# Performance work log

Hardware: AMD Instinct MI355X
Metric: run time of the kernel (lower is better)

Reference implementation:

```python
import jax, jax.numpy as jnp
import numpy as np

LAYERS = 2
HEADS = 4
TYPE_IDX = 1  # type='logic' -> 1
HIDDEN = 256
HEAD_DIM = HIDDEN // HEADS
EPS = 1e-6


def setup_inputs() -> dict:
    key = jax.random.key(0)
    ks = jax.random.split(key, 12)
    B, S, H = 4, 2048, HIDDEN
    inputs = jax.random.normal(ks[0], (B, S, H), jnp.float32)
    graphs = jax.random.uniform(ks[1], (B, 2, S, S), jnp.float32)
    biases_batch = jax.random.normal(ks[2], (B, 2, S, S), jnp.float32)
    s_h = 1.0 / np.sqrt(H).astype(np.float32)
    s_d = 1.0 / np.sqrt(HEAD_DIM).astype(np.float32)
    gc_w = jax.random.normal(ks[3], (LAYERS, H, H), jnp.float32) * s_h
    gc_b = jnp.zeros((LAYERS, H), jnp.float32)
    attn_w = jax.random.normal(ks[4], (LAYERS, HEAD_DIM, H), jnp.float32) * s_h  # conv1 (1x1) weight
    attn_a = jax.random.normal(ks[5], (LAYERS, HEAD_DIM), jnp.float32) * s_d     # conv2_1 (1x1) weight
    ln_a = jnp.ones((H,), jnp.float32)
    ln_b = jnp.zeros((H,), jnp.float32)
    w1 = jax.random.normal(ks[6], (H, H), jnp.float32) * s_h
    w1b = jnp.zeros((H,), jnp.float32)
    w2 = jax.random.normal(ks[7], (H, H), jnp.float32) * s_h
    w2b = jnp.zeros((H,), jnp.float32)
    return dict(inputs=inputs, graphs=graphs, biases_batch=biases_batch,
                gc_w=gc_w, gc_b=gc_b, attn_w=attn_w, attn_a=attn_a,
                ln_a=ln_a, ln_b=ln_b, w1=w1, w1b=w1b, w2=w2, w2b=w2b)


def reference(inputs, graphs, biases_batch, gc_w, gc_b, attn_w, attn_a, ln_a, ln_b, w1, w1b, w2, w2b):
    adj = graphs[:, TYPE_IDX]          # [b,s,s]
    bias = biases_batch[:, TYPE_IDX]   # [b,s,s]
    x0 = inputs
    x = inputs
    for i in range(LAYERS):
        # GraphConvolution: adj @ (x @ W) + b
        mf = jnp.einsum('bij,bjh->bih', adj, x @ gc_w[i]) + gc_b[i]
        # Node_Attn_head (NOTE: original uses conv2_1 for BOTH f_1 and f_2)
        seq_fts = jnp.einsum('bsh,dh->bsd', mf, attn_w[i])      # [b,s,d]
        f = seq_fts @ attn_a[i]                                  # [b,s]
        logits = jax.nn.leaky_relu(f[:, :, None] + f[:, None, :])  # f_2^T + f_1 -> [b,s,s]
        coefs = jax.nn.softmax(logits + bias, axis=1)            # Softmax(dim=1)
        ret = jax.nn.leaky_relu(jnp.einsum('bij,bjd->bid', coefs, seq_fts))  # [b,s,d]
        # shared attention head across all HEADS -> identical outputs, concatenated
        x = jnp.tile(ret, (1, 1, HEADS)) + x
    # LayerNorm (torch.std is unbiased -> ddof=1), residual to original inputs
    mean = x.mean(-1, keepdims=True)
    std = jnp.std(x, axis=-1, keepdims=True, ddof=1)
    g = ln_a * (x - mean) / (std + EPS) + ln_b + x0
    # PositionwiseFeedForward (dropout inactive in eval)
    ff = jax.nn.relu(g @ w1.T + w1b) @ w2.T + w2b
    return ff + g
```

## Files before the change

kernel.cpp:

```cpp
#include <hip/hip_runtime.h>
#include <math.h>

#define BB 4
#define SS 2048
#define HH 256
#define DD 64
#define NLAYERS 2
#define NPART 128

#define XSC  (1.f/64.f)
#define XSCI 64.f
#define FSC  (1.f/256.f)
#define WSC  256.f

typedef _Float16 f16;
typedef f16 half8 __attribute__((ext_vector_type(8)));
typedef f16 half4 __attribute__((ext_vector_type(4)));
typedef float f32x4 __attribute__((ext_vector_type(4)));
#define MFMA16(a, b, c) __builtin_amdgcn_mfma_f32_16x16x32_f16(a, b, c, 0, 0, 0)

__device__ __forceinline__ float lrelu(float v) { return v > 0.f ? v : 0.01f * v; }
__device__ __forceinline__ int enc(float f) { int i = __float_as_int(f); return i >= 0 ? i : (i ^ 0x7fffffff); }
__device__ __forceinline__ float dec(int k) { int i = k >= 0 ? k : (k ^ 0x7fffffff); return __int_as_float(i); }
__device__ __forceinline__ void split8(const float* v, half8& h, half8& l) {
    #pragma unroll
    for (int e = 0; e < 8; ++e) {
        f16 hh = (f16)v[e]; h[e] = hh; l[e] = (f16)((v[e] - (float)hh) * 2048.f);
    }
}

__global__ __launch_bounds__(256) void split_scale(
    const float* __restrict__ src, f16* __restrict__ dh, f16* __restrict__ dl, float scale)
{
    long i = ((long)blockIdx.x * 256 + threadIdx.x) * 8;
    float4 a = *(const float4*)&src[i];
    float4 b = *(const float4*)&src[i + 4];
    float v[8] = {a.x * scale, a.y * scale, a.z * scale, a.w * scale,
                  b.x * scale, b.y * scale, b.z * scale, b.w * scale};
    half8 h, l; split8(v, h, l);
    *(half8*)&dh[i] = h; *(half8*)&dl[i] = l;
}

__global__ __launch_bounds__(256) void prep_wy(
    const float* __restrict__ gc_w, const float* __restrict__ gc_b,
    const float* __restrict__ attn_w,
    f16* __restrict__ WysH, f16* __restrict__ WysL, float* __restrict__ by,
    const float* __restrict__ w1, const float* __restrict__ w2,
    f16* __restrict__ w1h, f16* __restrict__ w1l,
    f16* __restrict__ w2h, f16* __restrict__ w2l, int* __restrict__ FMXi)
{
    int L = blockIdx.x >> 6, d = blockIdx.x & 63;
    int h = threadIdx.x;
    const float* gw = gc_w + (long)L * HH * HH;
    const float* aw = attn_w + (long)L * DD * HH + (long)d * HH;
    float acc = 0.f;
    for (int hp = 0; hp < HH; ++hp) acc += gw[(long)h * HH + hp] * aw[hp];
    f16 hh = (f16)acc;
    WysH[((long)L * DD + d) * HH + h] = hh;
    WysL[((long)L * DD + d) * HH + h] = (f16)((acc - (float)hh) * 2048.f);
    if (h == 0) {
        float ba = 0.f;
        const float* gb = gc_b + (long)L * HH;
        for (int hp = 0; hp < HH; ++hp) ba += gb[hp] * aw[hp];
        by[L * DD + d] = ba;
    }
    int gt = blockIdx.x * 256 + h;
    #pragma unroll
    for (int p = 0; p < 4; ++p) {
        int e = gt * 4 + p;
        if (e < 65536) {
            float v = w1[e]; f16 x = (f16)v;
            w1h[e] = x; w1l[e] = (f16)((v - (float)x) * 2048.f);
        } else {
            int e2 = e - 65536;
            float v = w2[e2]; f16 x = (f16)v;
            w2h[e2] = x; w2l[e2] = (f16)((v - (float)x) * 2048.f);
        }
    }
    if (blockIdx.x == 0 && h < 2 * BB) FMXi[h] = enc(-1e30f);
}

__global__ __launch_bounds__(256) void y_mfma(
    const f16* __restrict__ xh, const f16* __restrict__ xl,
    const f16* __restrict__ WyhL, const f16* __restrict__ WylL,
    f16* __restrict__ yTh, f16* __restrict__ yTl)
{
    const int tid = threadIdx.x;
    const int w = tid >> 6, l = tid & 63;
    const int gw = blockIdx.x * 4 + w;
    const int b = gw >> 7, st = gw & 127;
    const int s0 = st * 16;
    const int lr = l & 15, kg = (l >> 4) * 8;
    const f16* Aph = xh + ((long)b * SS + s0 + lr) * HH;
    const f16* Apl = xl + ((long)b * SS + s0 + lr) * HH;
    f32x4 acch[4] = {}, accm[4] = {};
    #pragma unroll
    for (int k0 = 0; k0 < HH; k0 += 32) {
        half8 ah = *(const half8*)(Aph + k0 + kg);
        half8 al = *(const half8*)(Apl + k0 + kg);
        #pragma unroll
        for (int dt = 0; dt < 4; ++dt) {
            long boff = (long)(dt * 16 + lr) * HH + k0 + kg;
            half8 bh = *(const half8*)(WyhL + boff);
            half8 bl = *(const half8*)(WylL + boff);
            acch[dt] = MFMA16(ah, bh, acch[dt]);
            accm[dt] = MFMA16(ah, bl, accm[dt]);
            accm[dt] = MFMA16(al, bh, accm[dt]);
        }
    }
    const int rg0 = (l >> 4) * 4;
    #pragma unroll
    for (int dt = 0; dt < 4; ++dt) {
        int d = dt * 16 + lr;
        half4 h4, l4;
        #pragma unroll
        for (int rr = 0; rr < 4; ++rr) {
            float v = acch[dt][rr] + accm[dt][rr] * (1.f / 2048.f);
            f16 hh = (f16)v; h4[rr] = hh; l4[rr] = (f16)((v - (float)hh) * 2048.f);
        }
        long ob = ((long)b * DD + d) * SS + s0 + rg0;
        *(half4*)(yTh + ob) = h4;
        *(half4*)(yTl + ob) = l4;
    }
}

__global__ __launch_bounds__(512, 4) void ftp_fused(
    const float* __restrict__ adjB,
    const f16* __restrict__ yTh, const f16* __restrict__ yTl,
    const float* __restrict__ byL, const float* __restrict__ aaL,
    float* __restrict__ F, f16* __restrict__ fTh, f16* __restrict__ fTl,
    int* __restrict__ fmxSlot)
{
    __shared__ float Ls[8][16][68];
    __shared__ float fmaxS[16];
    const int b = blockIdx.y;
    const int i0 = blockIdx.x * 16;
    const int tid = threadIdx.x;
    const int w = tid >> 6, l = tid & 63, lr = l & 15, kg = (l >> 4) * 8;
    const float* Arow = adjB + (long)b * 2 * SS * SS + (long)(i0 + lr) * SS;
    const f16* Bh = yTh + ((long)b * DD + lr) * SS;
    const f16* Bl = yTl + ((long)b * DD + lr) * SS;

    f32x4 acch[4] = {}, accm[4] = {};
    #pragma unroll
    for (int ks = 0; ks < 256; ks += 32) {
        int k = w * 256 + ks + kg;
        float4 a0 = *(const float4*)(Arow + k);
        float4 a1 = *(const float4*)(Arow + k + 4);
        float av[8] = {a0.x, a0.y, a0.z, a0.w, a1.x, a1.y, a1.z, a1.w};
        half8 ah, al; split8(av, ah, al);
        #pragma unroll
        for (int dt = 0; dt < 4; ++dt) {
            long off = (long)dt * 16 * SS + k;
            half8 bh = *(const half8*)(Bh + off);
            half8 bl = *(const half8*)(Bl + off);
            acch[dt] = MFMA16(ah, bh, acch[dt]);
            accm[dt] = MFMA16(ah, bl, accm[dt]);
            accm[dt] = MFMA16(al, bh, accm[dt]);
        }
    }
    const int rg0 = (l >> 4) * 4;
    #pragma unroll
    for (int dt = 0; dt < 4; ++dt)
        #pragma unroll
        for (int rr = 0; rr < 4; ++rr)
            Ls[w][rg0 + rr][dt * 16 + lr] = acch[dt][rr] + accm[dt][rr] * (1.f / 2048.f);
    __syncthreads();

    {
        int r = tid >> 5, q = tid & 31, c0 = q * 2;
        float s0 = 0.f, s1 = 0.f;
        #pragma unroll
        for (int ww = 0; ww < 8; ++ww) { s0 += Ls[ww][r][c0]; s1 += Ls[ww][r][c0 + 1]; }
        s0 = s0 * XSCI + byL[c0];
        s1 = s1 * XSCI + byL[c0 + 1];
        Ls[0][r][c0] = s0; Ls[0][r][c0 + 1] = s1;
        float dot = s0 * aaL[c0] + s1 * aaL[c0 + 1];
        dot += __shfl_xor(dot, 1, 64);
        dot += __shfl_xor(dot, 2, 64);
        dot += __shfl_xor(dot, 4, 64);
        dot += __shfl_xor(dot, 8, 64);
        dot += __shfl_xor(dot, 16, 64);
        if (q == 0) { F[b * SS + i0 + r] = dot; fmaxS[r] = dot; }
    }
    __syncthreads();
    if (tid == 0) {
        float m = -1e30f;
        #pragma unroll
        for (int r = 0; r < 16; ++r) m = fmaxf(m, fmaxS[r]);
        atomicMax(fmxSlot + b, enc(m));
    }
    if (tid < 256) {
        int d = tid >> 2, sq = (tid & 3) * 4;
        half4 h4, l4;
        #pragma unroll
        for (int e = 0; e < 4; ++e) {
            float v = Ls[0][sq + e][d] * FSC;
            f16 hh = (f16)v; h4[e] = hh; l4[e] = (f16)((v - (float)hh) * 2048.f);
        }
        long ob = ((long)b * DD + d) * SS + i0 + sq;
        *(half4*)(fTh + ob) = h4;
        *(half4*)(fTl + ob) = l4;
    }
}

__global__ __launch_bounds__(512) void col_stats_part(
    const float* __restrict__ biasb, const float* __restrict__ f,
    const int* __restrict__ fmxSlot,
    float* __restrict__ partS, float* __restrict__ Mv)
{
    __shared__ float fs[32];
    const int b = blockIdx.z;
    const int chunk = blockIdx.y;
    const int half = threadIdx.x >> 8;
    const int t = threadIdx.x & 255;
    const int j0 = blockIdx.x * 1024 + t * 4;
    const float* bb = biasb + (long)b * 2 * SS * SS;
    const int ibase = chunk * 32 + half * 16;

    if (threadIdx.x < 32) fs[threadIdx.x] = f[b * SS + chunk * 32 + threadIdx.x];

    float fj[4], M[4], s[4] = {0.f, 0.f, 0.f, 0.f};
    const float fmx = dec(fmxSlot[b]);
    #pragma unroll
    for (int q = 0; q < 4; ++q) {
        fj[q] = f[b * SS + j0 + q];
        M[q] = lrelu(fmx + fj[q]) + 8.f;
    }
    __syncthreads();

    #pragma unroll
    for (int ii = 0; ii < 16; ii += 2) {
        float fi0 = fs[half * 16 + ii], fi1 = fs[half * 16 + ii + 1];
        float4 b0 = *(const float4*)&bb[(long)(ibase + ii) * SS + j0];
        float4 b1 = *(const float4*)&bb[(long)(ibase + ii + 1) * SS + j0];
        s[0] += __expf(lrelu(fi0 + fj[0]) + b0.x - M[0]);
        s[1] += __expf(lrelu(fi0 + fj[1]) + b0.y - M[1]);
        s[2] += __expf(lrelu(fi0 + fj[2]) + b0.z - M[2]);
        s[3] += __expf(lrelu(fi0 + fj[3]) + b0.w - M[3]);
        s[0] += __expf(lrelu(fi1 + fj[0]) + b1.x - M[0]);
        s[1] += __expf(lrelu(fi1 + fj[1]) + b1.y - M[1]);
        s[2] += __expf(lrelu(fi1 + fj[2]) + b1.z - M[2]);
        s[3] += __expf(lrelu(fi1 + fj[3]) + b1.w - M[3]);
    }
    const int c = chunk * 2 + half;
    #pragma unroll
    for (int q = 0; q < 4; ++q)
        partS[((long)c * BB + b) * SS + j0 + q] = s[q];
    if (chunk == 0 && half == 0) {
        #pragma unroll
        for (int q = 0; q < 4; ++q) Mv[b * SS + j0 + q] = M[q];
    }
}

__global__ __launch_bounds__(256) void col_stats_merge(
    const float* __restrict__ partS, float* __restrict__ Sinv)
{
    __shared__ float red[4][64];
    const int b = blockIdx.y;
    const int jl = threadIdx.x & 63;
    const int p = threadIdx.x >> 6;
    const int j = blockIdx.x * 64 + jl;
    float s = 0.f;
    #pragma unroll
    for (int k = 0; k < 32; ++k)
        s += partS[((long)(p * 32 + k) * BB + b) * SS + j];
    red[p][jl] = s;
    __syncthreads();
    if (p == 0) {
        float tot = ((red[0][jl] + red[1][jl]) + (red[2][jl] + red[3][jl]));
        Sinv[b * SS + j] = 1.f / tot;
    }
}

__global__ __launch_bounds__(512, 4) void pvp_fused(
    const float* __restrict__ biasb, const float* __restrict__ f,
    const float* __restrict__ Mv, const float* __restrict__ Sinv,
    const f16* __restrict__ fTh, const f16* __restrict__ fTl,
    const float* __restrict__ xin, float* __restrict__ X,
    f16* __restrict__ xh, f16* __restrict__ xl, int writeSplit)
{
    __shared__ float Ls[8][16][68];
    const int b = blockIdx.y;
    const int i0 = blockIdx.x * 16;
    const int tid = threadIdx.x;
    const int w = tid >> 6, l = tid & 63, lr = l & 15, kg = (l >> 4) * 8;
    const int irow = i0 + lr;
    const float fi = f[b * SS + irow];
    const float* brow = biasb + (long)b * 2 * SS * SS + (long)irow * SS;
    const float* fb = f + b * SS;
    const float* mb = Mv + b * SS;
    const float* sb = Sinv + b * SS;
    const f16* Bh = fTh + ((long)b * DD + lr) * SS;
    const f16* Bl = fTl + ((long)b * DD + lr) * SS;

    f32x4 acch[4] = {}, accm[4] = {};
    #pragma unroll
    for (int jc = 0; jc < 256; jc += 32) {
        const int jb = w * 256 + jc + kg;
        float4 bs0 = *(const float4*)(brow + jb);
        float4 bs1 = *(const float4*)(brow + jb + 4);
        float4 fj0 = *(const float4*)(fb + jb);
        float4 fj1 = *(const float4*)(fb + jb + 4);
        float4 mj0 = *(const float4*)(mb + jb);
        float4 mj1 = *(const float4*)(mb + jb + 4);
        float4 sj0 = *(const float4*)(sb + jb);
        float4 sj1 = *(const float4*)(sb + jb + 4);
        float wv[8];
        wv[0] = __expf(lrelu(fi + fj0.x) + bs0.x - mj0.x) * sj0.x * WSC;
        wv[1] = __expf(lrelu(fi + fj0.y) + bs0.y - mj0.y) * sj0.y * WSC;
        wv[2] = __expf(lrelu(fi + fj0.z) + bs0.z - mj0.z) * sj0.z * WSC;
        wv[3] = __expf(lrelu(fi + fj0.w) + bs0.w - mj0.w) * sj0.w * WSC;
        wv[4] = __expf(lrelu(fi + fj1.x) + bs1.x - mj1.x) * sj1.x * WSC;
        wv[5] = __expf(lrelu(fi + fj1.y) + bs1.y - mj1.y) * sj1.y * WSC;
        wv[6] = __expf(lrelu(fi + fj1.z) + bs1.z - mj1.z) * sj1.z * WSC;
        wv[7] = __expf(lrelu(fi + fj1.w) + bs1.w - mj1.w) * sj1.w * WSC;
        half8 ah, al; split8(wv, ah, al);
        #pragma unroll
        for (int dt = 0; dt < 4; ++dt) {
            long off = (long)dt * 16 * SS + jb;
            half8 bh = *(const half8*)(Bh + off);
            half8 bl = *(const half8*)(Bl + off);
            acch[dt] = MFMA16(ah, bh, acch[dt]);
            accm[dt] = MFMA16(ah, bl, accm[dt]);
            accm[dt] = MFMA16(al, bh, accm[dt]);
        }
    }
    const int rg0 = (l >> 4) * 4;
    #pragma unroll
    for (int dt = 0; dt < 4; ++dt)
        #pragma unroll
        for (int rr = 0; rr < 4; ++rr)
            Ls[w][rg0 + rr][dt * 16 + lr] = acch[dt][rr] + accm[dt][rr] * (1.f / 2048.f);
    __syncthreads();

    {
        int r = tid >> 5, q = tid & 31, dq = q * 2;
        float v0 = 0.f, v1 = 0.f;
        #pragma unroll
        for (int ww = 0; ww < 8; ++ww) { v0 += Ls[ww][r][dq]; v1 += Ls[ww][r][dq + 1]; }
        v0 = lrelu(v0); v1 = lrelu(v1);
        long rowoff = ((long)b * SS + i0 + r) * HH;
        #pragma unroll
        for (int rep = 0; rep < 4; ++rep) {
            long off = rowoff + rep * DD + dq;
            float o0 = v0 + xin[off];
            float o1 = v1 + xin[off + 1];
            X[off] = o0; X[off + 1] = o1;
            if (writeSplit) {
                float s0 = o0 * XSC, s1 = o1 * XSC;
                f16 h0 = (f16)s0, h1 = (f16)s1;
                xh[off] = h0; xl[off] = (f16)((s0 - (float)h0) * 2048.f);
                xh[off + 1] = h1; xl[off + 1] = (f16)((s1 - (float)h1) * 2048.f);
            }
        }
    }
}

__global__ __launch_bounds__(256) void layernorm_g(
    const float* __restrict__ x, const float* __restrict__ x0,
    const float* __restrict__ lna, const float* __restrict__ lnb,
    float* __restrict__ g, f16* __restrict__ gh, f16* __restrict__ gl)
{
    __shared__ float red[8];
    long row = blockIdx.x;
    int t = threadIdx.x;
    int wave = t >> 6, lane = t & 63;
    float v = x[row * HH + t];

    float sum = v;
    #pragma unroll
    for (int off = 32; off; off >>= 1) sum += __shfl_down(sum, off, 64);
    if (lane == 0) red[wave] = sum;
    __syncthreads();
    if (t < 64) {
        float s = (lane < 4) ? red[lane] : 0.f;
        s += __shfl_down(s, 2, 64);
        s += __shfl_down(s, 1, 64);
        if (lane == 0) red[4] = s / HH;
    }
    __syncthreads();
    float mean = red[4];
    float d = v - mean;
    float sq = d * d;
    #pragma unroll
    for (int off = 32; off; off >>= 1) sq += __shfl_down(sq, off, 64);
    __syncthreads();
    if (lane == 0) red[wave] = sq;
    __syncthreads();
    if (t < 64) {
        float s = (lane < 4) ? red[lane] : 0.f;
        s += __shfl_down(s, 2, 64);
        s += __shfl_down(s, 1, 64);
        if (lane == 0) red[5] = sqrtf(s / (HH - 1));
    }
    __syncthreads();
    float stdv = red[5];
    float gv = lna[t] * d / (stdv + 1e-6f) + lnb[t] + x0[row * HH + t];
    g[row * HH + t] = gv;
    f16 hh = (f16)gv;
    gh[row * HH + t] = hh;
    gl[row * HH + t] = (f16)((gv - (float)hh) * 2048.f);
}

__global__ __launch_bounds__(256) void ffn_mfma(
    const f16* __restrict__ Ah, const f16* __restrict__ Al,
    const f16* __restrict__ Bh, const f16* __restrict__ Bl,
    const float* __restrict__ bias, const float* __restrict__ res,
    float* __restrict__ outF, f16* __restrict__ outH, f16* __restrict__ outL,
    int doRelu)
{
    __shared__ float Ls[64][68];
    const int i0 = blockIdx.x * 64, j0 = blockIdx.y * 64;
    const int tid = threadIdx.x;
    const int w = tid >> 6, l = tid & 63, lr = l & 15, kg = (l >> 4) * 8;
    const f16* Aph = Ah + ((long)i0 + w * 16 + lr) * HH;
    const f16* Apl = Al + ((long)i0 + w * 16 + lr) * HH;
    f32x4 acch[4] = {}, accm[4] = {};
    #pragma unroll
    for (int k0 = 0; k0 < HH; k0 += 32) {
        half8 ah = *(const half8*)(Aph + k0 + kg);
        half8 al = *(const half8*)(Apl + k0 + kg);
        #pragma unroll
        for (int dt = 0; dt < 4; ++dt) {
            long boff = ((long)(j0 + dt * 16 + lr)) * HH + k0 + kg;
            half8 bh = *(const half8*)(Bh + boff);
            half8 bl = *(const half8*)(Bl + boff);
            acch[dt] = MFMA16(ah, bh, acch[dt]);
            accm[dt] = MFMA16(ah, bl, accm[dt]);
            accm[dt] = MFMA16(al, bh, accm[dt]);
        }
    }
    const int rg0 = (l >> 4) * 4;
    #pragma unroll
    for (int dt = 0; dt < 4; ++dt) {
        float bj = bias[j0 + dt * 16 + lr];
        #pragma unroll
        for (int rr = 0; rr < 4; ++rr) {
            float v = acch[dt][rr] + accm[dt][rr] * (1.f / 2048.f) + bj;
            if (doRelu) v = fmaxf(v, 0.f);
            Ls[w * 16 + rg0 + rr][dt * 16 + lr] = v;
        }
    }
    __syncthreads();
    int s = tid >> 2, nq = (tid & 3) * 16;
    long go = ((long)i0 + s) * HH + j0 + nq;
    if (outF) {
        #pragma unroll
        for (int q = 0; q < 4; ++q) {
            float4 v = *(float4*)&Ls[s][nq + q * 4];
            if (res) {
                float4 r = *(const float4*)&res[go + q * 4];
                v.x += r.x; v.y += r.y; v.z += r.z; v.w += r.w;
            }
            *(float4*)&outF[go + q * 4] = v;
        }
    } else {
        float v0[8], v1[8];
        #pragma unroll
        for (int e = 0; e < 8; ++e) { v0[e] = Ls[s][nq + e]; v1[e] = Ls[s][nq + 8 + e]; }
        half8 h0, l0, h1, l1; split8(v0, h0, l0); split8(v1, h1, l1);
        *(half8*)&outH[go] = h0; *(half8*)&outH[go + 8] = h1;
        *(half8*)&outL[go] = l0; *(half8*)&outL[go + 8] = l1;
    }
}

extern "C" void kernel_launch(void* const* d_in, const int* in_sizes, int n_in,
                              void* d_out, int out_size, void* d_ws, size_t ws_size,
                              hipStream_t stream)
{
    const float* inputs = (const float*)d_in[0];
    const float* graphs = (const float*)d_in[1];
    const float* biases = (const float*)d_in[2];
    const float* gc_w   = (const float*)d_in[3];
    const float* gc_b   = (const float*)d_in[4];
    const float* attn_w = (const float*)d_in[5];
    const float* attn_a = (const float*)d_in[6];
    const float* ln_a   = (const float*)d_in[7];
    const float* ln_b   = (const float*)d_in[8];
    const float* w1     = (const float*)d_in[9];
    const float* w1b    = (const float*)d_in[10];
    const float* w2     = (const float*)d_in[11];
    const float* w2b    = (const float*)d_in[12];
    float* out = (float*)d_out;

    float* ws   = (float*)d_ws;
    float* X    = ws;
    float* G    = ws + 2097152;
    float* PTS  = ws + 4194304;
    float* F    = ws + 5242880;
    float* Mv   = ws + 5251072;
    float* Sv   = ws + 5259264;
    float* by   = ws + 5267456;
    int*   FMXi = (int*)(ws + 5267584);
    f16* WysH   = (f16*)(ws + 5267712);
    f16* WysL   = (f16*)(ws + 5284096);
    f16* yTh    = (f16*)(ws + 5300480);
    f16* yTl    = (f16*)(ws + 5562624);
    f16* fTh    = (f16*)(ws + 5824768);
    f16* fTl    = (f16*)(ws + 6086912);
    f16* xh     = (f16*)(ws + 6349056);
    f16* xl     = (f16*)(ws + 7397632);
    f16* gh     = (f16*)(ws + 8446208);
    f16* gl     = (f16*)(ws + 9494784);
    f16* h1h    = (f16*)(ws + 10543360);
    f16* h1l    = (f16*)(ws + 11591936);
    f16* w1h    = (f16*)(ws + 12640512);
    f16* w1l    = (f16*)(ws + 12673280);
    f16* w2h    = (f16*)(ws + 12706048);
    f16* w2l    = (f16*)(ws + 12738816);

    const float* adjBase  = graphs + (long)SS * SS;
    const float* biasBase = biases + (long)SS * SS;

    prep_wy<<<128, 256, 0, stream>>>(gc_w, gc_b, attn_w, WysH, WysL, by,
                                     w1, w2, w1h, w1l, w2h, w2l, FMXi);
    split_scale<<<1024, 256, 0, stream>>>(inputs, xh, xl, XSC);

    for (int L = 0; L < NLAYERS; ++L) {
        y_mfma<<<128, 256, 0, stream>>>(xh, xl,
            WysH + (long)L * DD * HH, WysL + (long)L * DD * HH, yTh, yTl);
        ftp_fused<<<dim3(128, BB), 512, 0, stream>>>(
            adjBase, yTh, yTl, by + L * DD, attn_a + (long)L * DD,
            F, fTh, fTl, FMXi + L * BB);
        col_stats_part<<<dim3(2, 64, BB), 512, 0, stream>>>(
            biasBase, F, FMXi + L * BB, PTS, Mv);
        col_stats_merge<<<dim3(32, BB), 256, 0, stream>>>(PTS, Sv);
        pvp_fused<<<dim3(128, BB), 512, 0, stream>>>(
            biasBase, F, Mv, Sv, fTh, fTl,
            (L == 0) ? inputs : X, X, xh, xl, (L == 0) ? 1 : 0);
    }

    layernorm_g<<<BB * SS, 256, 0, stream>>>(X, inputs, ln_a, ln_b, G, gh, gl);
    ffn_mfma<<<dim3(128, 4), 256, 0, stream>>>(gh, gl, w1h, w1l, w1b,
                                               nullptr, nullptr, h1h, h1l, 1);
    ffn_mfma<<<dim3(128, 4), 256, 0, stream>>>(h1h, h1l, w2h, w2l, w2b,
                                               G, out, nullptr, nullptr, 0);
}
```

Before: 311.2 us.

## Fold softmax normalizer into log-space offset, wave-per-row layernorm, vectorize prep

The column max, the 1/sum and the fp16 scale are folded into a single per-column log-space offset (log 256 - log sum - max), so pvp_fused streams one vector instead of two and drops two multiplies per element. LayerNorm now handles one row per wavefront with float4 loads and xor shuffles, removing shared-memory reductions and barriers. prep_wy's dot product is vectorized with float4. The launch bounds of ftp_fused and pvp_fused drop from 4 to 2 blocks per CU, which gives the compiler more registers at the cost of occupancy.

Result: faster. 303.8 us (-2.4%).

```diff
diff --git a/kernel.cpp b/kernel.cpp
--- a/kernel.cpp
+++ b/kernel.cpp
@@ -12,6 +12,7 @@
 #define XSCI 64.f
 #define FSC  (1.f/256.f)
 #define WSC  256.f
+#define LNWSC 5.5451774444795624f
 
 typedef _Float16 f16;
 typedef f16 half8 __attribute__((ext_vector_type(8)));
@@ -51,10 +52,15 @@
 {
     int L = blockIdx.x >> 6, d = blockIdx.x & 63;
     int h = threadIdx.x;
-    const float* gw = gc_w + (long)L * HH * HH;
+    const float* gwr = gc_w + (long)L * HH * HH + (long)h * HH;
     const float* aw = attn_w + (long)L * DD * HH + (long)d * HH;
     float acc = 0.f;
-    for (int hp = 0; hp < HH; ++hp) acc += gw[(long)h * HH + hp] * aw[hp];
+    #pragma unroll 4
+    for (int hp = 0; hp < HH; hp += 4) {
+        float4 g4 = *(const float4*)&gwr[hp];
+        float4 a4 = *(const float4*)&aw[hp];
+        acc += g4.x * a4.x + g4.y * a4.y + g4.z * a4.z + g4.w * a4.w;
+    }
     f16 hh = (f16)acc;
     WysH[((long)L * DD + d) * HH + h] = hh;
     WysL[((long)L * DD + d) * HH + h] = (f16)((acc - (float)hh) * 2048.f);
@@ -124,7 +130,7 @@
     }
 }
 
-__global__ __launch_bounds__(512, 4) void ftp_fused(
+__global__ __launch_bounds__(512, 2) void ftp_fused(
     const float* __restrict__ adjB,
     const f16* __restrict__ yTh, const f16* __restrict__ yTl,
     const float* __restrict__ byL, const float* __restrict__ aaL,
@@ -254,7 +260,8 @@
 }
 
 __global__ __launch_bounds__(256) void col_stats_merge(
-    const float* __restrict__ partS, float* __restrict__ Sinv)
+    const float* __restrict__ partS, const float* __restrict__ Mv,
+    float* __restrict__ Cv)
 {
     __shared__ float red[4][64];
     const int b = blockIdx.y;
@@ -269,13 +276,13 @@
     __syncthreads();
     if (p == 0) {
         float tot = ((red[0][jl] + red[1][jl]) + (red[2][jl] + red[3][jl]));
-        Sinv[b * SS + j] = 1.f / tot;
-    }
-}
-
-__global__ __launch_bounds__(512, 4) void pvp_fused(
+        Cv[b * SS + j] = LNWSC - __logf(tot) - Mv[b * SS + j];
+    }
+}
+
+__global__ __launch_bounds__(512, 2) void pvp_fused(
     const float* __restrict__ biasb, const float* __restrict__ f,
-    const float* __restrict__ Mv, const float* __restrict__ Sinv,
+    const float* __restrict__ Cv,
     const f16* __restrict__ fTh, const f16* __restrict__ fTl,
     const float* __restrict__ xin, float* __restrict__ X,
     f16* __restrict__ xh, f16* __restrict__ xl, int writeSplit)
@@ -289,8 +296,7 @@
     const float fi = f[b * SS + irow];
     const float* brow = biasb + (long)b * 2 * SS * SS + (long)irow * SS;
     const float* fb = f + b * SS;
-    const float* mb = Mv + b * SS;
-    const float* sb = Sinv + b * SS;
+    const float* cb = Cv + b * SS;
     const f16* Bh = fTh + ((long)b * DD + lr) * SS;
     const f16* Bl = fTl + ((long)b * DD + lr) * SS;
 
@@ -302,19 +308,17 @@
         float4 bs1 = *(const float4*)(brow + jb + 4);
         float4 fj0 = *(const float4*)(fb + jb);
         float4 fj1 = *(const float4*)(fb + jb + 4);
-        float4 mj0 = *(const float4*)(mb + jb);
-        float4 mj1 = *(const float4*)(mb + jb + 4);
-        float4 sj0 = *(const float4*)(sb + jb);
-        float4 sj1 = *(const float4*)(sb + jb + 4);
+        float4 cj0 = *(const float4*)(cb + jb);
+        float4 cj1 = *(const float4*)(cb + jb + 4);
         float wv[8];
-        wv[0] = __expf(lrelu(fi + fj0.x) + bs0.x - mj0.x) * sj0.x * WSC;
-        wv[1] = __expf(lrelu(fi + fj0.y) + bs0.y - mj0.y) * sj0.y * WSC;
-        wv[2] = __expf(lrelu(fi + fj0.z) + bs0.z - mj0.z) * sj0.z * WSC;
-        wv[3] = __expf(lrelu(fi + fj0.w) + bs0.w - mj0.w) * sj0.w * WSC;
-        wv[4] = __expf(lrelu(fi + fj1.x) + bs1.x - mj1.x) * sj1.x * WSC;
-        wv[5] = __expf(lrelu(fi + fj1.y) + bs1.y - mj1.y) * sj1.y * WSC;
-        wv[6] = __expf(lrelu(fi + fj1.z) + bs1.z - mj1.z) * sj1.z * WSC;
-        wv[7] = __expf(lrelu(fi + fj1.w) + bs1.w - mj1.w) * sj1.w * WSC;
+        wv[0] = __expf(lrelu(fi + fj0.x) + bs0.x + cj0.x);
+        wv[1] = __expf(lrelu(fi + fj0.y) + bs0.y + cj0.y);
+        wv[2] = __expf(lrelu(fi + fj0.z) + bs0.z + cj0.z);
+        wv[3] = __expf(lrelu(fi + fj0.w) + bs0.w + cj0.w);
+        wv[4] = __expf(lrelu(fi + fj1.x) + bs1.x + cj1.x);
+        wv[5] = __expf(lrelu(fi + fj1.y) + bs1.y + cj1.y);
+        wv[6] = __expf(lrelu(fi + fj1.z) + bs1.z + cj1.z);
+        wv[7] = __expf(lrelu(fi + fj1.w) + bs1.w + cj1.w);
         half8 ah, al; split8(wv, ah, al);
         #pragma unroll
         for (int dt = 0; dt < 4; ++dt) {
@@ -362,45 +366,36 @@
     const float* __restrict__ lna, const float* __restrict__ lnb,
     float* __restrict__ g, f16* __restrict__ gh, f16* __restrict__ gl)
 {
-    __shared__ float red[8];
-    long row = blockIdx.x;
-    int t = threadIdx.x;
-    int wave = t >> 6, lane = t & 63;
-    float v = x[row * HH + t];
-
-    float sum = v;
-    #pragma unroll
-    for (int off = 32; off; off >>= 1) sum += __shfl_down(sum, off, 64);
-    if (lane == 0) red[wave] = sum;
-    __syncthreads();
-    if (t < 64) {
-        float s = (lane < 4) ? red[lane] : 0.f;
-        s += __shfl_down(s, 2, 64);
-        s += __shfl_down(s, 1, 64);
-        if (lane == 0) red[4] = s / HH;
-    }
-    __syncthreads();
-    float mean = red[4];
-    float d = v - mean;
-    float sq = d * d;
-    #pragma unroll
-    for (int off = 32; off; off >>= 1) sq += __shfl_down(sq, off, 64);
-    __syncthreads();
-    if (lane == 0) red[wave] = sq;
-    __syncthreads();
-    if (t < 64) {
-        float s = (lane < 4) ? red[lane] : 0.f;
-        s += __shfl_down(s, 2, 64);
-        s += __shfl_down(s, 1, 64);
-        if (lane == 0) red[5] = sqrtf(s / (HH - 1));
-    }
-    __syncthreads();
-    float stdv = red[5];
-    float gv = lna[t] * d / (stdv + 1e-6f) + lnb[t] + x0[row * HH + t];
-    g[row * HH + t] = gv;
-    f16 hh = (f16)gv;
-    gh[row * HH + t] = hh;
-    gl[row * HH + t] = (f16)((gv - (float)hh) * 2048.f);
+    const int wave = threadIdx.x >> 6, lane = threadIdx.x & 63;
+    const long row = (long)blockIdx.x * 4 + wave;
+    const int c0 = lane * 4;
+    float4 v = *(const float4*)&x[row * HH + c0];
+    float s = v.x + v.y + v.z + v.w;
+    #pragma unroll
+    for (int off = 32; off; off >>= 1) s += __shfl_xor(s, off, 64);
+    float mean = s * (1.f / HH);
+    float dx = v.x - mean, dy = v.y - mean, dz = v.z - mean, dw = v.w - mean;
+    float sq = dx * dx + dy * dy + dz * dz + dw * dw;
+    #pragma unroll
+    for (int off = 32; off; off >>= 1) sq += __shfl_xor(sq, off, 64);
+    float stdv = sqrtf(sq * (1.f / (HH - 1)));
+    float rinv = 1.f / (stdv + 1e-6f);
+    float4 la = *(const float4*)&lna[c0];
+    float4 lb = *(const float4*)&lnb[c0];
+    float4 xo = *(const float4*)&x0[row * HH + c0];
+    float gv[4];
+    gv[0] = la.x * dx * rinv + lb.x + xo.x;
+    gv[1] = la.y * dy * rinv + lb.y + xo.y;
+    gv[2] = la.z * dz * rinv + lb.z + xo.z;
+    gv[3] = la.w * dw * rinv + lb.w + xo.w;
+    *(float4*)&g[row * HH + c0] = *(float4*)gv;
+    half4 h4, l4;
+    #pragma unroll
+    for (int e = 0; e < 4; ++e) {
+        f16 hh = (f16)gv[e]; h4[e] = hh; l4[e] = (f16)((gv[e] - (float)hh) * 2048.f);
+    }
+    *(half4*)&gh[row * HH + c0] = h4;
+    *(half4*)&gl[row * HH + c0] = l4;
 }
 
 __global__ __launch_bounds__(256) void ffn_mfma(
@@ -490,7 +485,7 @@
     float* PTS  = ws + 4194304;
     float* F    = ws + 5242880;
     float* Mv   = ws + 5251072;
-    float* Sv   = ws + 5259264;
+    float* Cv   = ws + 5259264;
     float* by   = ws + 5267456;
     int*   FMXi = (int*)(ws + 5267584);
     f16* WysH   = (f16*)(ws + 5267712);
@@ -525,13 +520,13 @@
             F, fTh, fTl, FMXi + L * BB);
         col_stats_part<<<dim3(2, 64, BB), 512, 0, stream>>>(
             biasBase, F, FMXi + L * BB, PTS, Mv);
-        col_stats_merge<<<dim3(32, BB), 256, 0, stream>>>(PTS, Sv);
+        col_stats_merge<<<dim3(32, BB), 256, 0, stream>>>(PTS, Mv, Cv);
         pvp_fused<<<dim3(128, BB), 512, 0, stream>>>(
-            biasBase, F, Mv, Sv, fTh, fTl,
+            biasBase, F, Cv, fTh, fTl,
             (L == 0) ? inputs : X, X, xh, xl, (L == 0) ? 1 : 0);
     }
 
-    layernorm_g<<<BB * SS, 256, 0, stream>>>(X, inputs, ln_a, ln_b, G, gh, gl);
+    layernorm_g<<<2048, 256, 0, stream>>>(X, inputs, ln_a, ln_b, G, gh, gl);
     ffn_mfma<<<dim3(128, 4), 256, 0, stream>>>(gh, gl, w1h, w1l, w1b,
                                                nullptr, nullptr, h1h, h1l, 1);
     ffn_mfma<<<dim3(128, 4), 256, 0, stream>>>(h1h, h1l, w2h, w2l, w2b,
```
